# Kernel tuning notes

Hardware: AMD Instinct MI355X
Metric: run time of the kernel (lower is better)

The kernel has to match this reference:

```python
import jax, jax.numpy as jnp
import numpy as np

# SemiConv2d with semifield_type='MaxMin':
#   out[n,oc,i,j] = max_{ic,kh,kw} min(x_pad[n,ic,i+kh,j+kw], kernel[oc,ic,kh,kw])
# stride=1, 'same' padding with -inf (identity of max).

def setup_inputs() -> dict:
    key = jax.random.key(0)
    kx, kk = jax.random.split(key)
    x = jax.random.normal(kx, (8, 32, 96, 96), dtype=jnp.float32)
    kernel = jax.random.normal(kk, (32, 32, 3, 3), dtype=jnp.float32)
    return {"x": x, "kernel": kernel}


def reference(x, kernel):
    N, IC, H, W = x.shape
    OC, IC2, KH, KW = kernel.shape
    assert IC == IC2
    # same padding for k=3, stride=1 (left=top=1, right=bottom=1)
    p = KH - 1
    top = left = p // 2
    bot = right = p - top
    xp = jnp.pad(x, ((0, 0), (0, 0), (top, bot), (left, right)),
                 constant_values=-jnp.inf)
    out = None
    # small fixed loop over kernel taps (KH*KW = 9); vectorized over N, OC, IC, H, W
    for kh in range(KH):
        for kw in range(KW):
            win = xp[:, :, kh:kh + H, kw:kw + W]           # [N, IC, H, W]
            k_tap = kernel[:, :, kh, kw]                   # [OC, IC]
            # min over values, max over input channels -> [N, OC, H, W]
            v = jnp.max(jnp.minimum(win[:, None], k_tap[None, :, :, None, None]), axis=2)
            out = v if out is None else jnp.maximum(out, v)
    return out
```

## Files before the change

### kernel.cpp

```cpp
#include <hip/hip_runtime.h>
#include <math.h>
#include <stdint.h>


#define HH 96
#define WW 96
#define CIN 32
#define OCN 32
#define XQ_ROWS 98
#define XQ_W 48
#define XQ_SLICE (XQ_ROWS * XQ_W)
#define XQ_TOTAL (256 * XQ_SLICE)
#define TB_TOTAL (32 * 288)
#define WS_NEED ((size_t)XQ_TOTAL * 8 + (size_t)TB_TOTAL * 16)
#define NEGH2 0xFC00FC00u

typedef _Float16 h2 __attribute__((ext_vector_type(2)));
typedef uint32_t u2a4 __attribute__((ext_vector_type(2), aligned(4)));

__device__ __forceinline__ uint32_t pkmin_vs(uint32_t x, uint32_t k) {
    uint32_t d;
    asm("v_pk_min_f16 %0, %1, %2" : "=v"(d) : "v"(x), "s"(k));
    return d;
}
__device__ __forceinline__ uint32_t pkmin_vv(uint32_t a, uint32_t b) {
    uint32_t d;
    asm("v_pk_min_f16 %0, %1, %2" : "=v"(d) : "v"(a), "v"(b));
    return d;
}
__device__ __forceinline__ uint32_t pkmax(uint32_t a, uint32_t b) {
    uint32_t d;
    asm("v_pk_max_f16 %0, %1, %2" : "=v"(d) : "v"(a), "v"(b));
    return d;
}
__device__ __forceinline__ uint32_t packh2(float lo, float hi) {
    h2 p = {(_Float16)lo, (_Float16)hi};
    return __builtin_bit_cast(uint32_t, p);
}

__global__ __launch_bounds__(256) void setup_xq(const float* __restrict__ x,
                                                uint2* __restrict__ xq) {
    int idx = blockIdx.x * 256 + threadIdx.x;
    int j  = idx % XQ_W;
    int t  = idx / XQ_W;
    int hp = t % XQ_ROWS;
    int s  = t / XQ_ROWS;
    int h  = hp - 1;
    bool hv = (h >= 0) && (h < HH);
    const float* row = x + ((size_t)s * HH + (hv ? h : 0)) * WW;
    float a = (hv && j > 0)        ? row[2 * j - 1] : -INFINITY;
    float b = hv                   ? row[2 * j]     : -INFINITY;
    float c = hv                   ? row[2 * j + 1] : -INFINITY;
    float d = (hv && j < XQ_W - 1) ? row[2 * j + 2] : -INFINITY;
    uint2 v;
    v.x = packh2(a, b);
    v.y = packh2(c, d);
    xq[idx] = v;
}

__global__ void setup_tap(const float* __restrict__ kk, uint4* __restrict__ tbl) {
    __shared__ float ks[288];
    const int oc = blockIdx.x;
    const int t  = threadIdx.x;
    float k = kk[oc * 288 + t];
    ks[t] = k;
    __syncthreads();
    int rank = 0;
    for (int s = 0; s < 288; ++s) {
        float kv = ks[s];
        rank += (kv > k) || (kv == k && s < t);
    }
    const int ic = t / 9, tap = t % 9, dh = tap / 3, dw = tap % 3;
    uint32_t off = (uint32_t)(ic * XQ_ROWS + dh) * (XQ_W * 8) + (dw == 2 ? 4u : 0u);
    uint32_t sh  = (dw == 1) ? 16u : 0u;
    tbl[oc * 288 + rank] = make_uint4(packh2(k, k), off, sh, 0u);
}

__device__ __forceinline__ uint32_t tapval(const char* xb, int vbyte, uint4 e) {
    u2a4 q = *(const u2a4*)(xb + e.y + (uint32_t)vbyte);
    uint32_t v = __builtin_amdgcn_alignbit(q.y, q.x, e.z);
    return pkmin_vs(v, e.x);
}

__global__ __launch_bounds__(192, 8) void semiconv_ee(const char* __restrict__ xqb,
                                                      const uint4* __restrict__ tbl,
                                                      float* __restrict__ out) {
    const int tid = threadIdx.x;
    const int jj = tid % 48;
    const int hr = tid / 48;
    const int b  = blockIdx.x;
    const int hp = b % 24;
    const int t  = b / 24;
    const int oc = t & 31;
    const int n  = t >> 5;
    const int h  = hp * 4 + hr;

    const char* xb = xqb + (size_t)n * CIN * XQ_SLICE * 8;
    const int vbyte = (h * XQ_W + jj) * 8;
    const uint4* tb = tbl + oc * 288;

    uint32_t acc = NEGH2;
    uint4 e0 = tb[0], e1 = tb[1], e2 = tb[2], e3 = tb[3];

    for (int c = 0; c < 72; ++c) {
        uint4 f0, f1, f2, f3;
        if (c < 71) {
            const uint4* nb = tb + 4 * (c + 1);
            f0 = nb[0]; f1 = nb[1]; f2 = nb[2]; f3 = nb[3];
        }
        uint32_t m0 = tapval(xb, vbyte, e0);
        uint32_t m1 = tapval(xb, vbyte, e1);
        uint32_t m2 = tapval(xb, vbyte, e2);
        uint32_t m3 = tapval(xb, vbyte, e3);
        acc = pkmax(acc, pkmax(pkmax(m0, m1), pkmax(m2, m3)));

        if (c < 71) {
            uint32_t sw = __builtin_amdgcn_alignbit(acc, acc, 16);
            uint32_t mn = pkmin_vv(acc, sw);
            h2 a  = __builtin_bit_cast(h2, mn);
            h2 kn = __builtin_bit_cast(h2, f0.x);
            if (__all((float)a.x >= (float)kn.x)) break;
            e0 = f0; e1 = f1; e2 = f2; e3 = f3;
        }
    }

    h2 a = __builtin_bit_cast(h2, acc);
    float2 v = make_float2((float)a.x, (float)a.y);
    *(float2*)(out + (((size_t)(n * OCN + oc)) * HH + h) * WW + 2 * jj) = v;
}

#define NEGINF (-INFINITY)
__global__ __launch_bounds__(192, 8) void semiconv2d_f32(
    const float* __restrict__ x, const float* __restrict__ kk, float* __restrict__ out)
{
    const int tid = threadIdx.x;
    const int w  = tid % WW;
    const int hr = tid / WW;
    const int b   = blockIdx.x;
    const int ocb = b & 7;
    const int hp  = (b >> 3) % 48;
    const int n   = (b >> 3) / 48;
    const int h   = hp * 2 + hr;
    const int oc0 = ocb * 4;
    float a0[4], a1[4], a2[4];
#pragma unroll
    for (int i = 0; i < 4; ++i) { a0[i] = NEGINF; a1[i] = NEGINF; a2[i] = NEGINF; }
    const bool vm = (h > 0), vp = (h < HH - 1);
    const int hm  = vm ? h - 1 : h;
    const int hpl = vp ? h + 1 : h;
    const int cm  = (w > 0) ? -1 : 0;
    const int cp  = (w < WW - 1) ? 1 : 0;
    const float* rm = x + ((size_t)(n * CIN) * HH + hm)  * WW + w;
    const float* r1 = x + ((size_t)(n * CIN) * HH + h)   * WW + w;
    const float* rp = x + ((size_t)(n * CIN) * HH + hpl) * WW + w;
#pragma unroll 2
    for (int ic = 0; ic < CIN; ++ic) {
        float r00 = vm ? rm[cm] : NEGINF, r01 = vm ? rm[0] : NEGINF, r02 = vm ? rm[cp] : NEGINF;
        float r10 = r1[cm], r11 = r1[0], r12 = r1[cp];
        float r20 = vp ? rp[cm] : NEGINF, r21 = vp ? rp[0] : NEGINF, r22 = vp ? rp[cp] : NEGINF;
#pragma unroll
        for (int oc = 0; oc < 4; ++oc) {
            const float* kq = kk + (size_t)(((oc0 + oc) * CIN + ic)) * 9;
            a0[oc] = fmaxf(fmaxf(a0[oc], fminf(r00, kq[0])), fmaxf(fminf(r10, kq[3]), fminf(r20, kq[6])));
            a1[oc] = fmaxf(fmaxf(a1[oc], fminf(r01, kq[1])), fmaxf(fminf(r11, kq[4]), fminf(r21, kq[7])));
            a2[oc] = fmaxf(fmaxf(a2[oc], fminf(r02, kq[2])), fmaxf(fminf(r12, kq[5]), fminf(r22, kq[8])));
        }
        rm += HH * WW; r1 += HH * WW; rp += HH * WW;
    }
#pragma unroll
    for (int oc = 0; oc < 4; ++oc) {
        float v0 = (w > 0)      ? a0[oc] : NEGINF;
        float v2 = (w < WW - 1) ? a2[oc] : NEGINF;
        out[(((size_t)(n * OCN + oc0 + oc)) * HH + h) * WW + w] = fmaxf(fmaxf(v0, a1[oc]), v2);
    }
}

extern "C" void kernel_launch(void* const* d_in, const int* in_sizes, int n_in,
                              void* d_out, int out_size, void* d_ws, size_t ws_size,
                              hipStream_t stream) {
    const float* x  = (const float*)d_in[0];
    const float* kk = (const float*)d_in[1];
    float* out      = (float*)d_out;
    if (ws_size >= WS_NEED) {
        uint2* xq  = (uint2*)d_ws;
        uint4* tbl = (uint4*)((char*)d_ws + (size_t)XQ_TOTAL * 8);
        setup_xq<<<dim3(XQ_TOTAL / 256), dim3(256), 0, stream>>>(x, xq);
        setup_tap<<<dim3(32), dim3(288), 0, stream>>>(kk, tbl);
        semiconv_ee<<<dim3(8 * 32 * 24), dim3(192), 0, stream>>>(
            (const char*)xq, tbl, out);
    } else {
        semiconv2d_f32<<<dim3(8 * 48 * 8), dim3(192), 0, stream>>>(x, kk, out);
    }
}
```

Baseline: 101.6 us.

## Sort kernel rows instead of single taps for early-exit max-min convolution

The tap table moves from one entry per kernel tap (288, sorted by weight) to one entry per kernel row (96, sorted by the row's max weight). Each entry holds the three packed weights plus an offset, so one 8-byte load serves three taps and the per-tap shift lookup goes away. The early-exit test now compares the running minimum against the next row's max weight. Exit is coarser than per-tap sorting, so more work may run before the bound is met, in exchange for fewer loads and loop iterations per unit of work.

```diff
diff --git a/kernel.cpp b/kernel.cpp
--- a/kernel.cpp
+++ b/kernel.cpp
@@ -11,8 +11,10 @@
 #define XQ_W 48
 #define XQ_SLICE (XQ_ROWS * XQ_W)
 #define XQ_TOTAL (256 * XQ_SLICE)
-#define TB_TOTAL (32 * 288)
-#define WS_NEED ((size_t)XQ_TOTAL * 8 + (size_t)TB_TOTAL * 16)
+#define NROW 96
+#define TBL_BYTES ((size_t)32 * NROW * 16)
+#define RMX_BYTES ((size_t)32 * NROW * 4)
+#define WS_NEED ((size_t)XQ_TOTAL * 8 + TBL_BYTES + RMX_BYTES)
 #define NEGH2 0xFC00FC00u
 
 typedef _Float16 h2 __attribute__((ext_vector_type(2)));
@@ -58,33 +60,32 @@
     xq[idx] = v;
 }
 
-__global__ void setup_tap(const float* __restrict__ kk, uint4* __restrict__ tbl) {
-    __shared__ float ks[288];
+__global__ void setup_row(const float* __restrict__ kk, uint4* __restrict__ tbl,
+                          uint32_t* __restrict__ rmx) {
+    __shared__ float rs[NROW];
     const int oc = blockIdx.x;
     const int t  = threadIdx.x;
-    float k = kk[oc * 288 + t];
-    ks[t] = k;
+    const int ic = t / 3, dh = t - ic * 3;
+    const float* kp = kk + ((size_t)(oc * CIN + ic) * 3 + dh) * 3;
+    float k0 = kp[0], k1 = kp[1], k2 = kp[2];
+    float rm = fmaxf(fmaxf(k0, k1), k2);
+    rs[t] = rm;
     __syncthreads();
     int rank = 0;
-    for (int s = 0; s < 288; ++s) {
-        float kv = ks[s];
-        rank += (kv > k) || (kv == k && s < t);
-    }
-    const int ic = t / 9, tap = t % 9, dh = tap / 3, dw = tap % 3;
-    uint32_t off = (uint32_t)(ic * XQ_ROWS + dh) * (XQ_W * 8) + (dw == 2 ? 4u : 0u);
-    uint32_t sh  = (dw == 1) ? 16u : 0u;
-    tbl[oc * 288 + rank] = make_uint4(packh2(k, k), off, sh, 0u);
-}
-
-__device__ __forceinline__ uint32_t tapval(const char* xb, int vbyte, uint4 e) {
-    u2a4 q = *(const u2a4*)(xb + e.y + (uint32_t)vbyte);
-    uint32_t v = __builtin_amdgcn_alignbit(q.y, q.x, e.z);
-    return pkmin_vs(v, e.x);
-}
-
-__global__ __launch_bounds__(192, 8) void semiconv_ee(const char* __restrict__ xqb,
-                                                      const uint4* __restrict__ tbl,
-                                                      float* __restrict__ out) {
+    for (int s = 0; s < NROW; ++s) {
+        float v = rs[s];
+        rank += (v > rm) || (v == rm && s < t);
+    }
+    uint32_t off = (uint32_t)(ic * XQ_ROWS + dh) * (XQ_W * 8);
+    tbl[oc * NROW + rank] = make_uint4(packh2(k0, k0), packh2(k1, k1),
+                                       packh2(k2, k2), off);
+    rmx[oc * NROW + rank] = packh2(rm, rm);
+}
+
+__global__ __launch_bounds__(192, 8) void semiconv_row(const char* __restrict__ xqb,
+                                                       const uint4* __restrict__ tbl,
+                                                       const uint32_t* __restrict__ rmx,
+                                                       float* __restrict__ out) {
     const int tid = threadIdx.x;
     const int jj = tid % 48;
     const int hr = tid / 48;
@@ -95,32 +96,38 @@
     const int n  = t >> 5;
     const int h  = hp * 4 + hr;
 
-    const char* xb = xqb + (size_t)n * CIN * XQ_SLICE * 8;
-    const int vbyte = (h * XQ_W + jj) * 8;
-    const uint4* tb = tbl + oc * 288;
+    const char* xb = xqb + (size_t)n * CIN * XQ_SLICE * 8
+                         + (size_t)(h * XQ_W + jj) * 8;
+    const uint4* tb = tbl + oc * NROW;
+    const uint32_t* rb = rmx + oc * NROW;
 
     uint32_t acc = NEGH2;
-    uint4 e0 = tb[0], e1 = tb[1], e2 = tb[2], e3 = tb[3];
-
-    for (int c = 0; c < 72; ++c) {
-        uint4 f0, f1, f2, f3;
-        if (c < 71) {
-            const uint4* nb = tb + 4 * (c + 1);
-            f0 = nb[0]; f1 = nb[1]; f2 = nb[2]; f3 = nb[3];
+    uint4 e0 = tb[0], e1 = tb[1];
+
+    for (int c = 0; c < NROW / 2; ++c) {
+        uint4 f0, f1; uint32_t fr;
+        if (c < NROW / 2 - 1) {
+            const uint4* nb = tb + 2 * c + 2;
+            f0 = nb[0]; f1 = nb[1];
+            fr = rb[2 * c + 2];
         }
-        uint32_t m0 = tapval(xb, vbyte, e0);
-        uint32_t m1 = tapval(xb, vbyte, e1);
-        uint32_t m2 = tapval(xb, vbyte, e2);
-        uint32_t m3 = tapval(xb, vbyte, e3);
-        acc = pkmax(acc, pkmax(pkmax(m0, m1), pkmax(m2, m3)));
-
-        if (c < 71) {
+        u2a4 q0 = *(const u2a4*)(xb + e0.w);
+        u2a4 q1 = *(const u2a4*)(xb + e1.w);
+        uint32_t v01 = __builtin_amdgcn_alignbit(q0.y, q0.x, 16);
+        uint32_t v11 = __builtin_amdgcn_alignbit(q1.y, q1.x, 16);
+        uint32_t m0 = pkmax(pkmin_vs(q0.x, e0.x), pkmin_vs(v01, e0.y));
+        m0 = pkmax(m0, pkmin_vs(q0.y, e0.z));
+        uint32_t m1 = pkmax(pkmin_vs(q1.x, e1.x), pkmin_vs(v11, e1.y));
+        m1 = pkmax(m1, pkmin_vs(q1.y, e1.z));
+        acc = pkmax(acc, pkmax(m0, m1));
+
+        if (c < NROW / 2 - 1) {
             uint32_t sw = __builtin_amdgcn_alignbit(acc, acc, 16);
             uint32_t mn = pkmin_vv(acc, sw);
             h2 a  = __builtin_bit_cast(h2, mn);
-            h2 kn = __builtin_bit_cast(h2, f0.x);
+            h2 kn = __builtin_bit_cast(h2, fr);
             if (__all((float)a.x >= (float)kn.x)) break;
-            e0 = f0; e1 = f1; e2 = f2; e3 = f3;
+            e0 = f0; e1 = f1;
         }
     }
 
@@ -182,12 +189,13 @@
     const float* kk = (const float*)d_in[1];
     float* out      = (float*)d_out;
     if (ws_size >= WS_NEED) {
-        uint2* xq  = (uint2*)d_ws;
-        uint4* tbl = (uint4*)((char*)d_ws + (size_t)XQ_TOTAL * 8);
+        uint2*    xq  = (uint2*)d_ws;
+        uint4*    tbl = (uint4*)((char*)d_ws + (size_t)XQ_TOTAL * 8);
+        uint32_t* rmx = (uint32_t*)((char*)d_ws + (size_t)XQ_TOTAL * 8 + TBL_BYTES);
         setup_xq<<<dim3(XQ_TOTAL / 256), dim3(256), 0, stream>>>(x, xq);
-        setup_tap<<<dim3(32), dim3(288), 0, stream>>>(kk, tbl);
-        semiconv_ee<<<dim3(8 * 32 * 24), dim3(192), 0, stream>>>(
-            (const char*)xq, tbl, out);
+        setup_row<<<dim3(32), dim3(NROW), 0, stream>>>(kk, tbl, rmx);
+        semiconv_row<<<dim3(8 * 32 * 24), dim3(192), 0, stream>>>(
+            (const char*)xq, tbl, rmx, out);
     } else {
         semiconv2d_f32<<<dim3(8 * 48 * 8), dim3(192), 0, stream>>>(x, kk, out);
     }
```

Result: faster. 98.71 us (-2.8%).
